# Performance work log

Measured on AMD Instinct MI355X. Metric: run time of the kernel, lower is better.

The kernel has to match this reference:

```python
import jax, jax.numpy as jnp
import numpy as np

WIN = 11
SIGMA = 1.5
C1 = 0.01 ** 2
C2 = 0.03 ** 2


def _gauss1d():
    coords = jnp.arange(WIN, dtype=jnp.float32) - WIN // 2
    g = jnp.exp(-(coords ** 2) / (2.0 * SIGMA ** 2))
    return g / g.sum()


def _blur(x, g):
    C = x.shape[1]
    pad = WIN // 2
    dn = ('NCHW', 'OIHW', 'NCHW')
    kh = jnp.tile(g.reshape(1, 1, WIN, 1), (C, 1, 1, 1))
    kw = jnp.tile(g.reshape(1, 1, 1, WIN), (C, 1, 1, 1))
    x = jax.lax.conv_general_dilated(x, kh, (1, 1), ((pad, pad), (0, 0)),
                                     dimension_numbers=dn, feature_group_count=C)
    x = jax.lax.conv_general_dilated(x, kw, (1, 1), ((0, 0), (pad, pad)),
                                     dimension_numbers=dn, feature_group_count=C)
    return x


def _ssim_loss(pred, target, loss_weight=1.0):
    g = _gauss1d()
    mu1 = _blur(pred, g)
    mu2 = _blur(target, g)
    mu1_sq = mu1 * mu1
    mu2_sq = mu2 * mu2
    mu1_mu2 = mu1 * mu2
    sigma1_sq = _blur(pred * pred, g) - mu1_sq
    sigma2_sq = _blur(target * target, g) - mu2_sq
    sigma12 = _blur(pred * target, g) - mu1_mu2
    ssim_map = ((2.0 * mu1_mu2 + C1) * (2.0 * sigma12 + C2)) / \
               ((mu1_sq + mu2_sq + C1) * (sigma1_sq + sigma2_sq + C2))
    # size_average=True -> scalar mean; reduction='mean' on a scalar is identity
    return loss_weight * (1.0 - ssim_map.mean())


def setup_inputs() -> dict:
    key = jax.random.key(0)
    k1, k2 = jax.random.split(key)
    shape = (16, 3, 512, 512)
    pred = jax.random.uniform(k1, shape, dtype=jnp.float32)
    target = jax.random.uniform(k2, shape, dtype=jnp.float32)
    return {"pred": pred, "target": target}


def reference(pred, target):
    return _ssim_loss(pred, target, loss_weight=1.0)
```

## Files before the change

### kernel.cpp

```cpp
#include <hip/hip_runtime.h>

typedef float f2 __attribute__((ext_vector_type(2)));

#define IMG 512
#define TW 32
#define TH 32
#define NG 12
#define SROW 148
#define BOFFD 96
#define RROW 43
#define RS 52
#define N_TOT (16 * 3 * 512 * 512)
#define NBLK (256 * 48)
#define NSLOT 1024

__device__ __constant__ f2 Gw2[11] = {
    {0.00102838f, 0.00102838f}, {0.00759876f, 0.00759876f},
    {0.03600077f, 0.03600077f}, {0.10936086f, 0.10936086f},
    {0.21300537f, 0.21300537f}, {0.26601173f, 0.26601173f},
    {0.21300537f, 0.21300537f}, {0.10936086f, 0.10936086f},
    {0.03600077f, 0.03600077f}, {0.00759876f, 0.00759876f},
    {0.00102838f, 0.00102838f}};

__device__ __forceinline__ unsigned pkh(float a, float b) {
    unsigned r;
    asm("v_cvt_pkrtz_f16_f32 %0, %1, %2" : "=v"(r) : "v"(a), "v"(b));
    return r;
}
__device__ __forceinline__ f2 uph(unsigned u) {
    float lo, hi;
    const unsigned uh = u >> 16;
    asm("v_cvt_f32_f16 %0, %1" : "=v"(lo) : "v"(u));
    asm("v_cvt_f32_f16 %0, %1" : "=v"(hi) : "v"(uh));
    return (f2){lo, hi};
}

__device__ __forceinline__ void vtaps(const float4 P, const float4 T, const int k,
                                      f2 A0[4][2], f2 A1[4][2]) {
    const f2 p[2] = {{P.x, P.y}, {P.z, P.w}};
    const f2 t[2] = {{T.x, T.y}, {T.z, T.w}};
#pragma unroll
    for (int h = 0; h < 2; ++h) {
        const f2 ss = p[h] * p[h] + t[h] * t[h];
        const f2 pt = p[h] * t[h];
        if (k < 11) {
            const f2 w = Gw2[k];
            A0[0][h] += w * p[h];
            A0[1][h] += w * t[h];
            A0[2][h] += w * ss;
            A0[3][h] += w * pt;
        }
        if (k > 0) {
            const f2 w = Gw2[k - 1];
            A1[0][h] += w * p[h];
            A1[1][h] += w * t[h];
            A1[2][h] += w * ss;
            A1[3][h] += w * pt;
        }
    }
}

__global__ __launch_bounds__(256, 4) void ssim_main(const float* __restrict__ pred,
                                                    const float* __restrict__ tgt,
                                                    float* __restrict__ ws,
                                                    int parts_mode) {
    __shared__ __align__(16) float raw[2][RROW][RS];
    __shared__ __align__(16) float plane[TH * SROW];
    __shared__ float red[4];

    const int tid = threadIdx.x;
    const int plane_id = blockIdx.y;

    const int bx = blockIdx.x;
    const int tile = ((bx & 7) << 5) | (bx >> 3);
    const int tile_x = tile & 15;
    const int tile_y = tile >> 4;
    const int tx = tile_x * TW;
    const int ty = tile_y * TH;
    const float* pbase = pred + (size_t)plane_id * (IMG * IMG);
    const float* tbase = tgt + (size_t)plane_id * (IMG * IMG);

    {
        const bool interior = ((unsigned)(tile_x - 1) < 14u) && ((unsigned)(tile_y - 1) < 14u);
        if (interior) {
            for (int idx = tid; idx < 2 * RROW * NG; idx += 256) {
                const int arr = idx >= RROW * NG;
                const int j = idx - arr * (RROW * NG);
                const int r = j / NG;
                const int g = j - r * NG;
                const float* src = arr ? tbase : pbase;
                const float4 V = *(const float4*)(src + (ty + r - 5) * IMG + (tx + (g << 2) - 8));
                *(float4*)&raw[arr][r][g << 2] = V;
            }
        } else {
            for (int idx = tid; idx < 2 * RROW * NG; idx += 256) {
                const int arr = idx >= RROW * NG;
                const int j = idx - arr * (RROW * NG);
                const int r = j / NG;
                const int g = j - r * NG;
                const int y = ty + r - 5;
                const int x = tx + (g << 2) - 8;
                float4 V = make_float4(0.f, 0.f, 0.f, 0.f);
                if ((unsigned)y < (unsigned)IMG && (unsigned)x < (unsigned)IMG) {
                    const float* src = arr ? tbase : pbase;
                    V = *(const float4*)(src + y * IMG + x);
                }
                *(float4*)&raw[arr][r][g << 2] = V;
            }
        }
    }
    __syncthreads();

    if (tid < NG * 16) {
        const int g4 = tid % NG;
        const int rp = tid / NG;
        const int r0 = rp * 2;
        const int cb = g4 << 2;

        f2 A0[4][2], A1[4][2];
#pragma unroll
        for (int q = 0; q < 4; ++q)
#pragma unroll
            for (int h = 0; h < 2; ++h) { A0[q][h] = (f2)0.f; A1[q][h] = (f2)0.f; }

#pragma unroll
        for (int k = 0; k < 12; ++k) {
            const float4 P = *(const float4*)&raw[0][r0 + k][cb];
            const float4 T = *(const float4*)&raw[1][r0 + k][cb];
            vtaps(P, T, k, A0, A1);
        }

#pragma unroll
        for (int r = 0; r < 2; ++r) {
            f2 (*A)[2] = r ? A1 : A0;
            float* rowA = &plane[(r0 + r) * SROW + (cb << 1)];
            *(float4*)rowA       = make_float4(A[0][0].x, A[1][0].x, A[0][0].y, A[1][0].y);
            *(float4*)(rowA + 4) = make_float4(A[0][1].x, A[1][1].x, A[0][1].y, A[1][1].y);
            uint4 bv;
            bv.x = pkh(A[2][0].x, A[3][0].x);
            bv.y = pkh(A[2][0].y, A[3][0].y);
            bv.z = pkh(A[2][1].x, A[3][1].x);
            bv.w = pkh(A[2][1].y, A[3][1].y);
            *(uint4*)&plane[(r0 + r) * SROW + BOFFD + cb] = bv;
        }
    }
    __syncthreads();

    float lsum = 0.f;
    {
        const int oy = tid >> 3;
        const int ox = (tid & 7) << 2;
        const float* rowbase = &plane[oy * SROW];

        f2 acc[4];
        f2 sacc[4];
#pragma unroll
        for (int j = 0; j < 4; ++j) { acc[j] = (f2)0.f; sacc[j] = (f2)0.f; }

        {
            const float4* rowA = (const float4*)(rowbase + ((ox + 2) << 1));
#pragma unroll
            for (int i4 = 0; i4 < 8; ++i4) {
                const float4 q = rowA[i4];
                const f2 v[2] = {{q.x, q.y}, {q.z, q.w}};
#pragma unroll
                for (int h = 0; h < 2; ++h) {
                    const int i = 2 * i4 + h;
#pragma unroll
                    for (int j = 0; j < 4; ++j) {
                        const int k = i - 1 - j;
                        if (k >= 0 && k <= 10) acc[j] += Gw2[k] * v[h];
                    }
                }
            }
        }

        {
            const uint4* rowB = (const uint4*)(rowbase + BOFFD + ox);
#pragma unroll
            for (int i4 = 0; i4 < 5; ++i4) {
                const uint4 q = rowB[i4];
                const unsigned qq[4] = {q.x, q.y, q.z, q.w};
#pragma unroll
                for (int c = 0; c < 4; ++c) {
                    const int m = 4 * i4 + c;
                    if (m >= 3 && m <= 16) {
                        const f2 v = uph(qq[c]);
#pragma unroll
                        for (int j = 0; j < 4; ++j) {
                            const int k = m - 3 - j;
                            if (k >= 0 && k <= 10) sacc[j] += Gw2[k] * v;
                        }
                    }
                }
            }
        }

        const float C1 = 0.0001f;
        const float C2 = 0.0009f;
#pragma unroll
        for (int j = 0; j < 4; ++j) {
            const float m1 = acc[j].x, m2 = acc[j].y;
            const float bss = sacc[j].x, bpt = sacc[j].y;
            const float mu1s = m1 * m1;
            const float mu2s = m2 * m2;
            const float mu12 = m1 * m2;
            const float A = mu1s + mu2s;
            const float s12 = bpt - mu12;
            const float sden = bss - A;
            const float num = fmaf(2.f, mu12, C1) * fmaf(2.f, s12, C2);
            const float den = (A + C1) * (sden + C2);
            lsum += num * __builtin_amdgcn_rcpf(den);
        }
    }

#pragma unroll
    for (int off = 32; off > 0; off >>= 1) lsum += __shfl_down(lsum, off, 64);
    if ((tid & 63) == 0) red[tid >> 6] = lsum;
    __syncthreads();
    if (tid == 0) {
        const float bs = (red[0] + red[1]) + (red[2] + red[3]);
        const int bid = blockIdx.y * gridDim.x + blockIdx.x;
        if (parts_mode) {
            ws[bid] = bs;
        } else {
            atomicAdd(&ws[bid & (NSLOT - 1)], bs);
        }
    }
}

__global__ __launch_bounds__(1024) void ssim_final(const float4* __restrict__ ws4,
                                                   float* __restrict__ out, int count4) {
    __shared__ float red[16];
    const int tid = threadIdx.x;
    float s = 0.f;
    for (int i = tid; i < count4; i += 1024) {
        const float4 w = ws4[i];
        s += (w.x + w.y) + (w.z + w.w);
    }
#pragma unroll
    for (int off = 32; off > 0; off >>= 1) s += __shfl_down(s, off, 64);
    if ((tid & 63) == 0) red[tid >> 6] = s;
    __syncthreads();
    if (tid == 0) {
        float tot = 0.f;
#pragma unroll
        for (int i = 0; i < 16; ++i) tot += red[i];
        out[0] = 1.0f - tot * (1.0f / (float)N_TOT);
    }
}

extern "C" void kernel_launch(void* const* d_in, const int* in_sizes, int n_in,
                              void* d_out, int out_size, void* d_ws, size_t ws_size,
                              hipStream_t stream) {
    const float* pred = (const float*)d_in[0];
    const float* tgt = (const float*)d_in[1];
    float* out = (float*)d_out;
    float* ws = (float*)d_ws;

    const int parts_mode = (ws_size >= (size_t)NBLK * sizeof(float)) ? 1 : 0;
    if (!parts_mode) {
        hipMemsetAsync(ws, 0, NSLOT * sizeof(float), stream);
    }
    dim3 grid(256, 48);
    ssim_main<<<grid, 256, 0, stream>>>(pred, tgt, ws, parts_mode);
    ssim_final<<<1, 1024, 0, stream>>>((const float4*)ws, out,
                                       (parts_mode ? NBLK : NSLOT) / 4);
}
```

Measured before the change: 164.3 us.

## Stage raw tiles as packed fp16 and run vertical blur with packed-half FMAs

Inputs are converted to packed fp16 (pred,target pairs) while loading into shared memory, which halves raw staging LDS and its reads. The vertical Gaussian pass then uses v_pk_fma_f16/v_pk_mul_f16 on packed pairs, getting squares and cross products via a rotate trick, and accumulates in fp16 before unpacking. This cuts VALU instruction count and shared memory footprint, which may raise occupancy. The cost is reduced precision: fp16 accumulation of the moment sums risks accuracy loss in the sigma terms.

After: 159.1 us. -3.2%, faster.

```diff
diff --git a/kernel.cpp b/kernel.cpp
--- a/kernel.cpp
+++ b/kernel.cpp
@@ -9,7 +9,7 @@
 #define SROW 148
 #define BOFFD 96
 #define RROW 43
-#define RS 52
+#define RS16 52
 #define N_TOT (16 * 3 * 512 * 512)
 #define NBLK (256 * 48)
 #define NSLOT 1024
@@ -22,6 +22,10 @@
     {0.03600077f, 0.03600077f}, {0.00759876f, 0.00759876f},
     {0.00102838f, 0.00102838f}};
 
+__device__ __constant__ unsigned Gh2u[11] = {
+    0x14371437u, 0x1FC81FC8u, 0x289C289Cu, 0x2F002F00u, 0x32D132D1u, 0x34423442u,
+    0x32D132D1u, 0x2F002F00u, 0x289C289Cu, 0x1FC81FC8u, 0x14371437u};
+
 __device__ __forceinline__ unsigned pkh(float a, float b) {
     unsigned r;
     asm("v_cvt_pkrtz_f16_f32 %0, %1, %2" : "=v"(r) : "v"(a), "v"(b));
@@ -34,37 +38,30 @@
     asm("v_cvt_f32_f16 %0, %1" : "=v"(hi) : "v"(uh));
     return (f2){lo, hi};
 }
-
-__device__ __forceinline__ void vtaps(const float4 P, const float4 T, const int k,
-                                      f2 A0[4][2], f2 A1[4][2]) {
-    const f2 p[2] = {{P.x, P.y}, {P.z, P.w}};
-    const f2 t[2] = {{T.x, T.y}, {T.z, T.w}};
-#pragma unroll
-    for (int h = 0; h < 2; ++h) {
-        const f2 ss = p[h] * p[h] + t[h] * t[h];
-        const f2 pt = p[h] * t[h];
-        if (k < 11) {
-            const f2 w = Gw2[k];
-            A0[0][h] += w * p[h];
-            A0[1][h] += w * t[h];
-            A0[2][h] += w * ss;
-            A0[3][h] += w * pt;
-        }
-        if (k > 0) {
-            const f2 w = Gw2[k - 1];
-            A1[0][h] += w * p[h];
-            A1[1][h] += w * t[h];
-            A1[2][h] += w * ss;
-            A1[3][h] += w * pt;
-        }
-    }
+__device__ __forceinline__ unsigned pkmul(unsigned a, unsigned b) {
+    unsigned r;
+    asm("v_pk_mul_f16 %0, %1, %2" : "=v"(r) : "v"(a), "v"(b));
+    return r;
+}
+__device__ __forceinline__ unsigned pkfma(unsigned a, unsigned b, unsigned c) {
+    unsigned r;
+    asm("v_pk_fma_f16 %0, %1, %2, %3" : "=v"(r) : "v"(a), "v"(b), "v"(c));
+    return r;
+}
+__device__ __forceinline__ unsigned rot16(unsigned q) {
+    return (q >> 16) | (q << 16);
+}
+__device__ __forceinline__ unsigned mkB(unsigned aD, unsigned aP) {
+    const f2 d = uph(aD);
+    const f2 p = uph(aP);
+    return pkh(d.x + d.y, p.x);
 }
 
 __global__ __launch_bounds__(256, 4) void ssim_main(const float* __restrict__ pred,
                                                     const float* __restrict__ tgt,
                                                     float* __restrict__ ws,
                                                     int parts_mode) {
-    __shared__ __align__(16) float raw[2][RROW][RS];
+    __shared__ __align__(16) unsigned raw16[RROW * RS16];
     __shared__ __align__(16) float plane[TH * SROW];
     __shared__ float red[4];
 
@@ -83,29 +80,30 @@
     {
         const bool interior = ((unsigned)(tile_x - 1) < 14u) && ((unsigned)(tile_y - 1) < 14u);
         if (interior) {
-            for (int idx = tid; idx < 2 * RROW * NG; idx += 256) {
-                const int arr = idx >= RROW * NG;
-                const int j = idx - arr * (RROW * NG);
-                const int r = j / NG;
-                const int g = j - r * NG;
-                const float* src = arr ? tbase : pbase;
-                const float4 V = *(const float4*)(src + (ty + r - 5) * IMG + (tx + (g << 2) - 8));
-                *(float4*)&raw[arr][r][g << 2] = V;
+            for (int idx = tid; idx < RROW * NG; idx += 256) {
+                const int r = idx / NG;
+                const int g = idx - r * NG;
+                const int gx = (ty + r - 5) * IMG + (tx + (g << 2) - 8);
+                const float4 P = *(const float4*)(pbase + gx);
+                const float4 T = *(const float4*)(tbase + gx);
+                *(uint4*)&raw16[r * RS16 + (g << 2)] =
+                    make_uint4(pkh(P.x, T.x), pkh(P.y, T.y), pkh(P.z, T.z), pkh(P.w, T.w));
             }
         } else {
-            for (int idx = tid; idx < 2 * RROW * NG; idx += 256) {
-                const int arr = idx >= RROW * NG;
-                const int j = idx - arr * (RROW * NG);
-                const int r = j / NG;
-                const int g = j - r * NG;
+            for (int idx = tid; idx < RROW * NG; idx += 256) {
+                const int r = idx / NG;
+                const int g = idx - r * NG;
                 const int y = ty + r - 5;
                 const int x = tx + (g << 2) - 8;
-                float4 V = make_float4(0.f, 0.f, 0.f, 0.f);
+                float4 P = make_float4(0.f, 0.f, 0.f, 0.f);
+                float4 T = make_float4(0.f, 0.f, 0.f, 0.f);
                 if ((unsigned)y < (unsigned)IMG && (unsigned)x < (unsigned)IMG) {
-                    const float* src = arr ? tbase : pbase;
-                    V = *(const float4*)(src + y * IMG + x);
-                }
-                *(float4*)&raw[arr][r][g << 2] = V;
+                    const int gx = y * IMG + x;
+                    P = *(const float4*)(pbase + gx);
+                    T = *(const float4*)(tbase + gx);
+                }
+                *(uint4*)&raw16[r * RS16 + (g << 2)] =
+                    make_uint4(pkh(P.x, T.x), pkh(P.y, T.y), pkh(P.z, T.z), pkh(P.w, T.w));
             }
         }
     }
@@ -117,31 +115,51 @@
         const int r0 = rp * 2;
         const int cb = g4 << 2;
 
-        f2 A0[4][2], A1[4][2];
-#pragma unroll
-        for (int q = 0; q < 4; ++q)
-#pragma unroll
-            for (int h = 0; h < 2; ++h) { A0[q][h] = (f2)0.f; A1[q][h] = (f2)0.f; }
+        unsigned aA0[4], aA1[4], aD0[4], aD1[4], aP0[4], aP1[4];
+#pragma unroll
+        for (int j = 0; j < 4; ++j) {
+            aA0[j] = 0u; aA1[j] = 0u; aD0[j] = 0u;
+            aD1[j] = 0u; aP0[j] = 0u; aP1[j] = 0u;
+        }
 
 #pragma unroll
         for (int k = 0; k < 12; ++k) {
-            const float4 P = *(const float4*)&raw[0][r0 + k][cb];
-            const float4 T = *(const float4*)&raw[1][r0 + k][cb];
-            vtaps(P, T, k, A0, A1);
-        }
-
-#pragma unroll
-        for (int r = 0; r < 2; ++r) {
-            f2 (*A)[2] = r ? A1 : A0;
-            float* rowA = &plane[(r0 + r) * SROW + (cb << 1)];
-            *(float4*)rowA       = make_float4(A[0][0].x, A[1][0].x, A[0][0].y, A[1][0].y);
-            *(float4*)(rowA + 4) = make_float4(A[0][1].x, A[1][1].x, A[0][1].y, A[1][1].y);
-            uint4 bv;
-            bv.x = pkh(A[2][0].x, A[3][0].x);
-            bv.y = pkh(A[2][0].y, A[3][0].y);
-            bv.z = pkh(A[2][1].x, A[3][1].x);
-            bv.w = pkh(A[2][1].y, A[3][1].y);
-            *(uint4*)&plane[(r0 + r) * SROW + BOFFD + cb] = bv;
+            const uint4 Q = *(const uint4*)&raw16[(r0 + k) * RS16 + cb];
+            const unsigned q[4] = {Q.x, Q.y, Q.z, Q.w};
+#pragma unroll
+            for (int j = 0; j < 4; ++j) {
+                const unsigned d = pkmul(q[j], q[j]);
+                const unsigned e = pkmul(q[j], rot16(q[j]));
+                if (k < 11) {
+                    aA0[j] = pkfma(Gh2u[k], q[j], aA0[j]);
+                    aD0[j] = pkfma(Gh2u[k], d, aD0[j]);
+                    aP0[j] = pkfma(Gh2u[k], e, aP0[j]);
+                }
+                if (k > 0) {
+                    aA1[j] = pkfma(Gh2u[k - 1], q[j], aA1[j]);
+                    aD1[j] = pkfma(Gh2u[k - 1], d, aD1[j]);
+                    aP1[j] = pkfma(Gh2u[k - 1], e, aP1[j]);
+                }
+            }
+        }
+
+        {
+            const f2 m0 = uph(aA0[0]), m1 = uph(aA0[1]), m2 = uph(aA0[2]), m3 = uph(aA0[3]);
+            float* rowA = &plane[r0 * SROW + (cb << 1)];
+            *(float4*)rowA       = make_float4(m0.x, m0.y, m1.x, m1.y);
+            *(float4*)(rowA + 4) = make_float4(m2.x, m2.y, m3.x, m3.y);
+            *(uint4*)&plane[r0 * SROW + BOFFD + cb] =
+                make_uint4(mkB(aD0[0], aP0[0]), mkB(aD0[1], aP0[1]),
+                           mkB(aD0[2], aP0[2]), mkB(aD0[3], aP0[3]));
+        }
+        {
+            const f2 m0 = uph(aA1[0]), m1 = uph(aA1[1]), m2 = uph(aA1[2]), m3 = uph(aA1[3]);
+            float* rowA = &plane[(r0 + 1) * SROW + (cb << 1)];
+            *(float4*)rowA       = make_float4(m0.x, m0.y, m1.x, m1.y);
+            *(float4*)(rowA + 4) = make_float4(m2.x, m2.y, m3.x, m3.y);
+            *(uint4*)&plane[(r0 + 1) * SROW + BOFFD + cb] =
+                make_uint4(mkB(aD1[0], aP1[0]), mkB(aD1[1], aP1[1]),
+                           mkB(aD1[2], aP1[2]), mkB(aD1[3], aP1[3]));
         }
     }
     __syncthreads();
```
